# Kernel tuning notes

Measured on AMD Instinct MI355X. Metric: run time of the kernel, lower is better.

The kernel has to match this reference:

```python
import jax, jax.numpy as jnp
import numpy as np

D_KEY = 128
INF = 1e9  # stands in for the module's global INF constant


def setup_inputs() -> dict:
    key = jax.random.key(0)
    kq, kk, kv = jax.random.split(key, 3)
    B, S, D = 8, 4096, D_KEY
    return {
        "query": jax.random.normal(kq, (B, S, D), dtype=jnp.float32),
        "keys": jax.random.normal(kk, (B, S, D), dtype=jnp.float32),
        "values": jax.random.normal(kv, (B, S, D), dtype=jnp.float32),
    }


def reference(query, keys, values):
    # dot_products: [B, Sq, Sk]
    scores = jnp.einsum("bqd,bkd->bqk", query, keys)
    S = scores.shape[-1]
    # causal: subtract INF on strict upper triangle (triu(1)), applied BEFORE scaling
    causal = jnp.triu(jnp.ones((S, S), dtype=scores.dtype), 1) * INF
    logits = (scores - causal[None, :, :]) / jnp.asarray(np.sqrt(D_KEY), scores.dtype)
    # legacy F.softmax on 3D transposed tensor == softmax over key axis
    probs = jax.nn.softmax(logits, axis=-1)
    # dropout with p=0.0 is identity
    return jnp.einsum("bqk,bkd->bqd", probs, values)
```

## Files before the change

kernel.cpp:

```cpp
#include <hip/hip_runtime.h>
#include <hip/hip_bf16.h>

#define B_SZ   8
#define S_LEN  4096
#define D_K    128
#define KB     64
#define CH     16
#define NCHUNK 1280

#define KT_STR 136
#define VT_STR 72
#define PT_STR 72

typedef short  short8  __attribute__((ext_vector_type(8)));
typedef float  floatx4 __attribute__((ext_vector_type(4)));

#define EXP2F(x) exp2f(x)

__device__ __forceinline__ unsigned bfround(float x) {
  unsigned u = __builtin_bit_cast(unsigned, x);
  return (u + 0x7fffu + ((u >> 16) & 1u)) >> 16;
}
__device__ __forceinline__ unsigned bfpack2(float a, float b) {
  return bfround(a) | (bfround(b) << 16);
}


__global__ __launch_bounds__(256)
void conv_k(const float* __restrict__ K, unsigned short* __restrict__ Kb) {
  const size_t idx = ((size_t)blockIdx.x * 256 + threadIdx.x) * 8;
  float4 f0 = *(const float4*)(K + idx);
  float4 f1 = *(const float4*)(K + idx + 4);
  uint4 u;
  u.x = bfpack2(f0.x, f0.y);
  u.y = bfpack2(f0.z, f0.w);
  u.z = bfpack2(f1.x, f1.y);
  u.w = bfpack2(f1.z, f1.w);
  *(uint4*)(Kb + idx) = u;
}

__global__ __launch_bounds__(256)
void transp_v(const float* __restrict__ V, unsigned short* __restrict__ Vt) {
  __shared__ float tile[64][65];
  const int t   = threadIdx.x;
  const int bid = blockIdx.x;
  const int b   = bid >> 7;
  const int rem = bid & 127;
  const int kt  = (rem >> 1) * 64;
  const int dt  = (rem & 1) * 64;
  {
    const int c  = (t & 15) * 4;
    const int r0 = t >> 4;
#pragma unroll
    for (int rr = 0; rr < 4; ++rr) {
      const int r = r0 + rr * 16;
      float4 f = *(const float4*)(V + (size_t)(b * S_LEN + kt + r) * D_K + dt + c);
      tile[r][c]     = f.x;
      tile[r][c + 1] = f.y;
      tile[r][c + 2] = f.z;
      tile[r][c + 3] = f.w;
    }
  }
  __syncthreads();
  {
    const int d  = t >> 2;
    const int k0 = (t & 3) * 16;
#pragma unroll
    for (int j = 0; j < 16; j += 8) {
      uint4 u;
      u.x = bfpack2(tile[k0 + j + 0][d], tile[k0 + j + 1][d]);
      u.y = bfpack2(tile[k0 + j + 2][d], tile[k0 + j + 3][d]);
      u.z = bfpack2(tile[k0 + j + 4][d], tile[k0 + j + 5][d]);
      u.w = bfpack2(tile[k0 + j + 6][d], tile[k0 + j + 7][d]);
      *(uint4*)(Vt + (size_t)(b * D_K + dt + d) * S_LEN + kt + k0 + j) = u;
    }
  }
}

__global__ void zero_cnt(int* cnt) { *cnt = 0; }


__global__ __launch_bounds__(128, 2)
void attn_worker(const float* __restrict__ Q, const unsigned short* __restrict__ Kb,
                 const unsigned short* __restrict__ Vt, int* __restrict__ cnt,
                 float* __restrict__ ml, float* __restrict__ pO) {
  __shared__ __align__(16) short Klds[KB * KT_STR];
  __shared__ __align__(16) short Vtlds[D_K * VT_STR];
  __shared__ __align__(16) short Plds[2 * 16 * PT_STR];
  __shared__ int s_chunk;

  const int tid  = threadIdx.x;
  const int lane = tid & 63;
  const int w    = tid >> 6;
  const int l15  = lane & 15;
  const int quad = lane >> 4;

  const int kr0 = tid >> 4;
  const int kc  = (tid & 15) * 8;
  const int vr0 = tid >> 3;
  const int vc  = (tid & 7) * 8;

  const float CSC = 0.12752041f;

  for (;;) {
    if (tid == 0) s_chunk = atomicAdd(cnt, 1);
    __syncthreads();
    const int c = s_chunk;
    if (c >= NCHUNK) break;

    int b, qi, j;
    if (c < 800) {
      const int r = c >> 3;  b = c & 7;
      if      (r <  4) { qi = 63;               j = r;            }
      else if (r < 52) { qi = 62 - (r-4)/3;     j = (r-4)%3;      }
      else if (r < 84) { qi = 46 - (r-52)/2;    j = (r-52)%2;     }
      else             { qi = 30 - (r-84);      j = 0;            }
    } else {
      const int rc = c - 800;
      const int s  = 15 - (rc >> 5);
      const int t  = rc & 31;
      b  = t & 7;
      qi = s - 1 + 16 * (t >> 3);
      j  = (qi + 1) >> 4;
    }

    const int q0 = qi * 64;
    const int s0 = j * CH;
    const int s1 = min(s0 + CH, qi + 1);

    short8 bq[2][4];
    int qg[2];
#pragma unroll
    for (int sub = 0; sub < 2; ++sub) {
      qg[sub] = q0 + w * 32 + sub * 16 + l15;
      const float* qrow = Q + (size_t)(b * S_LEN + qg[sub]) * D_K + quad * 8;
#pragma unroll
      for (int kd = 0; kd < 4; ++kd) {
        float4 f0 = *(const float4*)(qrow + kd * 32);
        float4 f1 = *(const float4*)(qrow + kd * 32 + 4);
        union { short8 s; unsigned u[4]; } t;
        t.u[0] = bfpack2(f0.x, f0.y);
        t.u[1] = bfpack2(f0.z, f0.w);
        t.u[2] = bfpack2(f1.x, f1.y);
        t.u[3] = bfpack2(f1.z, f1.w);
        bq[sub][kd] = t.s;
      }
    }

    floatx4 acc[2][8];
#pragma unroll
    for (int sub = 0; sub < 2; ++sub)
#pragma unroll
      for (int nc = 0; nc < 8; ++nc) acc[sub][nc] = (floatx4){0.f, 0.f, 0.f, 0.f};
    float m_run[2] = {-1e30f, -1e30f}, l_run[2] = {0.f, 0.f};

    const unsigned short* kbase = Kb + (size_t)(b * S_LEN) * D_K;
    const unsigned short* vbase = Vt + (size_t)(b * D_K) * S_LEN;

    for (int s = s0; s < s1; ++s) {
      const int kt = s * KB;

#pragma unroll
      for (int i = 0; i < 8; ++i) {
        uint4 u = *(const uint4*)(kbase + (size_t)(kt + kr0 + i * 8) * D_K + kc);
        *(uint4*)(&Klds[(kr0 + i * 8) * KT_STR + kc]) = u;
      }
#pragma unroll
      for (int i = 0; i < 8; ++i) {
        uint4 u = *(const uint4*)(vbase + (size_t)(vr0 + i * 16) * S_LEN + kt + vc);
        *(uint4*)(&Vtlds[(vr0 + i * 16) * VT_STR + vc]) = u;
      }
      __syncthreads();

      floatx4 st[2][4];
#pragma unroll
      for (int kf = 0; kf < 4; ++kf) {
        floatx4 c0 = (floatx4){0.f, 0.f, 0.f, 0.f};
        floatx4 c1 = (floatx4){0.f, 0.f, 0.f, 0.f};
#pragma unroll
        for (int kd = 0; kd < 4; ++kd) {
          short8 a = *(const short8*)(&Klds[(kf * 16 + l15) * KT_STR + kd * 32 + quad * 8]);
          c0 = __builtin_amdgcn_mfma_f32_16x16x32_bf16(a, bq[0][kd], c0, 0, 0, 0);
          c1 = __builtin_amdgcn_mfma_f32_16x16x32_bf16(a, bq[1][kd], c1, 0, 0, 0);
        }
        st[0][kf] = c0;
        st[1][kf] = c1;
      }

      if (s == qi) {
#pragma unroll
        for (int sub = 0; sub < 2; ++sub)
#pragma unroll
          for (int kf = 0; kf < 4; ++kf)
#pragma unroll
            for (int r = 0; r < 4; ++r) {
              int key = kt + kf * 16 + quad * 4 + r;
              if (key > qg[sub]) st[sub][kf][r] = -1e30f;
            }
      }

      short8 pa[2][2];
#pragma unroll
      for (int sub = 0; sub < 2; ++sub) {
        float mx = st[sub][0][0];
#pragma unroll
        for (int kf = 0; kf < 4; ++kf)
#pragma unroll
          for (int r = 0; r < 4; ++r) mx = fmaxf(mx, st[sub][kf][r]);
        mx = fmaxf(mx, __shfl_xor(mx, 16, 64));
        mx = fmaxf(mx, __shfl_xor(mx, 32, 64));
        const float m_new = fmaxf(m_run[sub], mx);
        const float alpha = EXP2F((m_run[sub] - m_new) * CSC);

        float p[4][4];
        float tsum = 0.f;
#pragma unroll
        for (int kf = 0; kf < 4; ++kf)
#pragma unroll
          for (int r = 0; r < 4; ++r) {
            p[kf][r] = EXP2F((st[sub][kf][r] - m_new) * CSC);
            tsum += p[kf][r];
          }
        tsum += __shfl_xor(tsum, 16, 64);
        tsum += __shfl_xor(tsum, 32, 64);
        l_run[sub] = l_run[sub] * alpha + tsum;
        m_run[sub] = m_new;

#pragma unroll
        for (int r = 0; r < 4; ++r) {
          const float ar = __shfl(alpha, quad * 4 + r, 64);
#pragma unroll
          for (int nc = 0; nc < 8; ++nc) acc[sub][nc][r] *= ar;
        }

        short* pw = &Plds[(w * 16 + l15) * PT_STR];
#pragma unroll
        for (int kf = 0; kf < 4; ++kf) {
          uint2 u;
          u.x = bfpack2(p[kf][0], p[kf][1]);
          u.y = bfpack2(p[kf][2], p[kf][3]);
          *(uint2*)(&pw[kf * 16 + quad * 4]) = u;
        }
        __asm__ __volatile__("" ::: "memory");
        pa[sub][0] = *(const short8*)(&pw[quad * 8]);
        pa[sub][1] = *(const short8*)(&pw[32 + quad * 8]);
        __asm__ __volatile__("" ::: "memory");
      }

#pragma unroll
      for (int nc = 0; nc < 8; ++nc) {
        short8 bv0 = *(const short8*)(&Vtlds[(nc * 16 + l15) * VT_STR + quad * 8]);
        short8 bv1 = *(const short8*)(&Vtlds[(nc * 16 + l15) * VT_STR + 32 + quad * 8]);
        acc[0][nc] = __builtin_amdgcn_mfma_f32_16x16x32_bf16(pa[0][0], bv0, acc[0][nc], 0, 0, 0);
        acc[0][nc] = __builtin_amdgcn_mfma_f32_16x16x32_bf16(pa[0][1], bv1, acc[0][nc], 0, 0, 0);
        acc[1][nc] = __builtin_amdgcn_mfma_f32_16x16x32_bf16(pa[1][0], bv0, acc[1][nc], 0, 0, 0);
        acc[1][nc] = __builtin_amdgcn_mfma_f32_16x16x32_bf16(pa[1][1], bv1, acc[1][nc], 0, 0, 0);
      }
      __syncthreads();
    }

    const int slot = ((b << 6) | qi) * 4 + j;
    float* po = pO + (size_t)slot * 8192;
#pragma unroll
    for (int sub = 0; sub < 2; ++sub) {
#pragma unroll
      for (int r = 0; r < 4; ++r) {
        const int qrow = w * 32 + sub * 16 + quad * 4 + r;
        float* op = po + qrow * D_K + l15;
#pragma unroll
        for (int nc = 0; nc < 8; ++nc) op[nc * 16] = acc[sub][nc][r];
      }
      if (quad == 0) {
        const int qrow = w * 32 + sub * 16 + l15;
        ml[(size_t)slot * 128 + qrow * 2]     = m_run[sub];
        ml[(size_t)slot * 128 + qrow * 2 + 1] = l_run[sub];
      }
    }
  }
}


__global__ __launch_bounds__(256)
void attn_combine(const float* __restrict__ ml, const float* __restrict__ pO,
                  float* __restrict__ O) {
  const int t   = blockIdx.x;
  const int b   = t >> 6;
  const int qi  = t & 63;
  const int ncb = ((qi + 1) + 15) >> 4;
  const float CSC = 0.12752041f;

  const int tid = threadIdx.x;
  const int q   = tid >> 2;
  const int dp  = (tid & 3) * 32;

  float m[4], l[4];
  float M = -1e30f;
  for (int jj = 0; jj < ncb; ++jj) {
    const int slot = t * 4 + jj;
    m[jj] = ml[(size_t)slot * 128 + q * 2];
    l[jj] = ml[(size_t)slot * 128 + q * 2 + 1];
    M = fmaxf(M, m[jj]);
  }
  float wgt[4], L = 0.f;
  for (int jj = 0; jj < ncb; ++jj) {
    wgt[jj] = EXP2F((m[jj] - M) * CSC);
    L += wgt[jj] * l[jj];
  }
  const float inv = 1.0f / L;

  float4 out[8];
#pragma unroll
  for (int v = 0; v < 8; ++v) out[v] = make_float4(0.f, 0.f, 0.f, 0.f);
  for (int jj = 0; jj < ncb; ++jj) {
    const float* src = pO + (size_t)(t * 4 + jj) * 8192 + q * D_K + dp;
    const float wj = wgt[jj];
#pragma unroll
    for (int v = 0; v < 8; ++v) {
      float4 f = *(const float4*)(src + v * 4);
      out[v].x += wj * f.x;  out[v].y += wj * f.y;
      out[v].z += wj * f.z;  out[v].w += wj * f.w;
    }
  }
  float* dst = O + (size_t)(b * S_LEN + qi * 64 + q) * D_K + dp;
#pragma unroll
  for (int v = 0; v < 8; ++v) {
    float4 f = make_float4(out[v].x * inv, out[v].y * inv, out[v].z * inv, out[v].w * inv);
    *(float4*)(dst + v * 4) = f;
  }
}


__global__ __launch_bounds__(256, 2)
void attn_fwd_fb(const float* __restrict__ Q, const float* __restrict__ K,
                 const float* __restrict__ V, float* __restrict__ O) {
  __shared__ __align__(16) short Klds[KB * KT_STR];
  __shared__ __align__(16) short Vtlds[D_K * VT_STR];
  __shared__ __align__(16) short Plds[4 * 16 * PT_STR];

  const int tid  = threadIdx.x;
  const int lane = tid & 63;
  const int w    = tid >> 6;
  const int l15  = lane & 15;
  const int quad = lane >> 4;

  const int bid = blockIdx.x;
  const int b   = bid & 7;
  const int qi  = 63 - (bid >> 3);
  const int q0  = qi * 64;

  const float CSC = 0.12752041f;

  const int    qg   = q0 + w * 16 + l15;
  const float* qrow = Q + (size_t)(b * S_LEN + qg) * D_K + quad * 8;
  short8 bq[4];
#pragma unroll
  for (int kd = 0; kd < 4; ++kd) {
    float4 f0 = *(const float4*)(qrow + kd * 32);
    float4 f1 = *(const float4*)(qrow + kd * 32 + 4);
    union { short8 s; unsigned u[4]; } t;
    t.u[0] = bfpack2(f0.x, f0.y);
    t.u[1] = bfpack2(f0.z, f0.w);
    t.u[2] = bfpack2(f1.x, f1.y);
    t.u[3] = bfpack2(f1.z, f1.w);
    bq[kd] = t.s;
  }

  floatx4 acc[8];
#pragma unroll
  for (int nc = 0; nc < 8; ++nc) acc[nc] = (floatx4){0.f, 0.f, 0.f, 0.f};
  float m_run = -1e30f, l_run = 0.f;

  const int d4 = tid & 31;
  const int kq = tid >> 5;
  const int nsteps = qi + 1;

  for (int s = 0; s < nsteps; ++s) {
    const int kt = s * KB;
#pragma unroll
    for (int r2 = 0; r2 < 2; ++r2) {
      const int row = r2 * 32 + kq * 4;
      const float* kp = K + (size_t)(b * S_LEN + kt + row) * D_K + d4 * 4;
      const float* vp = V + (size_t)(b * S_LEN + kt + row) * D_K + d4 * 4;
      float4 fk[4], fv[4];
#pragma unroll
      for (int i = 0; i < 4; ++i) {
        fk[i] = *(const float4*)(kp + i * D_K);
        fv[i] = *(const float4*)(vp + i * D_K);
      }
#pragma unroll
      for (int i = 0; i < 4; ++i) {
        uint2 u;
        u.x = bfpack2(fk[i].x, fk[i].y);
        u.y = bfpack2(fk[i].z, fk[i].w);
        *(uint2*)(&Klds[(row + i) * KT_STR + d4 * 4]) = u;
      }
#pragma unroll
      for (int c = 0; c < 4; ++c) {
        float e0 = ((const float*)&fv[0])[c];
        float e1 = ((const float*)&fv[1])[c];
        float e2 = ((const float*)&fv[2])[c];
        float e3 = ((const float*)&fv[3])[c];
        uint2 u;
        u.x = bfpack2(e0, e1);
        u.y = bfpack2(e2, e3);
        *(uint2*)(&Vtlds[(d4 * 4 + c) * VT_STR + row]) = u;
      }
    }
    __syncthreads();

    floatx4 st[4];
#pragma unroll
    for (int kf = 0; kf < 4; ++kf) {
      floatx4 c = (floatx4){0.f, 0.f, 0.f, 0.f};
#pragma unroll
      for (int kd = 0; kd < 4; ++kd) {
        short8 a = *(const short8*)(&Klds[(kf * 16 + l15) * KT_STR + kd * 32 + quad * 8]);
        c = __builtin_amdgcn_mfma_f32_16x16x32_bf16(a, bq[kd], c, 0, 0, 0);
      }
      st[kf] = c;
    }

    if (s == nsteps - 1) {
#pragma unroll
      for (int kf = 0; kf < 4; ++kf)
#pragma unroll
        for (int r = 0; r < 4; ++r) {
          int key = kt + kf * 16 + quad * 4 + r;
          if (key > qg) st[kf][r] = -1e30f;
        }
    }

    float mx = st[0][0];
#pragma unroll
    for (int kf = 0; kf < 4; ++kf)
#pragma unroll
      for (int r = 0; r < 4; ++r) mx = fmaxf(mx, st[kf][r]);
    mx = fmaxf(mx, __shfl_xor(mx, 16, 64));
    mx = fmaxf(mx, __shfl_xor(mx, 32, 64));
    const float m_new = fmaxf(m_run, mx);
    const float alpha = EXP2F((m_run - m_new) * CSC);

    float p[4][4];
    float tsum = 0.f;
#pragma unroll
    for (int kf = 0; kf < 4; ++kf)
#pragma unroll
      for (int r = 0; r < 4; ++r) {
        p[kf][r] = EXP2F((st[kf][r] - m_new) * CSC);
        tsum += p[kf][r];
      }
    tsum += __shfl_xor(tsum, 16, 64);
    tsum += __shfl_xor(tsum, 32, 64);
    l_run = l_run * alpha + tsum;
    m_run = m_new;

#pragma unroll
    for (int r = 0; r < 4; ++r) {
      const float ar = __shfl(alpha, quad * 4 + r, 64);
#pragma unroll
      for (int nc = 0; nc < 8; ++nc) acc[nc][r] *= ar;
    }

    short* pw = &Plds[(w * 16 + l15) * PT_STR];
#pragma unroll
    for (int kf = 0; kf < 4; ++kf) {
      uint2 u;
      u.x = bfpack2(p[kf][0], p[kf][1]);
      u.y = bfpack2(p[kf][2], p[kf][3]);
      *(uint2*)(&pw[kf * 16 + quad * 4]) = u;
    }
    __asm__ __volatile__("" ::: "memory");
    short8 pa0 = *(const short8*)(&pw[quad * 8]);
    short8 pa1 = *(const short8*)(&pw[32 + quad * 8]);

#pragma unroll
    for (int nc = 0; nc < 8; ++nc) {
      short8 bv0 = *(const short8*)(&Vtlds[(nc * 16 + l15) * VT_STR + quad * 8]);
      acc[nc] = __builtin_amdgcn_mfma_f32_16x16x32_bf16(pa0, bv0, acc[nc], 0, 0, 0);
      short8 bv1 = *(const short8*)(&Vtlds[(nc * 16 + l15) * VT_STR + 32 + quad * 8]);
      acc[nc] = __builtin_amdgcn_mfma_f32_16x16x32_bf16(pa1, bv1, acc[nc], 0, 0, 0);
    }
    __syncthreads();
  }

#pragma unroll
  for (int r = 0; r < 4; ++r) {
    const float lr  = __shfl(l_run, quad * 4 + r, 64);
    const float inv = 1.0f / lr;
    const int qout  = q0 + w * 16 + quad * 4 + r;
    float* op = O + (size_t)(b * S_LEN + qout) * D_K + l15;
#pragma unroll
    for (int nc = 0; nc < 8; ++nc) op[nc * 16] = acc[nc][r] * inv;
  }
}


extern "C" void kernel_launch(void* const* d_in, const int* in_sizes, int n_in,
                              void* d_out, int out_size, void* d_ws, size_t ws_size,
                              hipStream_t stream) {
  const float* Q = (const float*)d_in[0];
  const float* K = (const float*)d_in[1];
  const float* V = (const float*)d_in[2];
  float* O = (float*)d_out;

  const size_t elems = (size_t)B_SZ * S_LEN * D_K;

  const size_t off_ml = 256;
  const size_t off_po = off_ml + 2048ull * 128 * 4;
  const size_t off_kb = off_po + 2048ull * 8192 * 4;
  const size_t off_vt = off_kb + elems * 2;
  const size_t need   = off_vt + elems * 2;

  if (ws_size >= need) {
    char* ws = (char*)d_ws;
    int*            cnt = (int*)ws;
    float*          ml  = (float*)(ws + off_ml);
    float*          po  = (float*)(ws + off_po);
    unsigned short* Kb  = (unsigned short*)(ws + off_kb);
    unsigned short* Vt  = (unsigned short*)(ws + off_vt);

    zero_cnt<<<dim3(1), dim3(1), 0, stream>>>(cnt);
    conv_k<<<dim3((unsigned)(elems / 8 / 256)), dim3(256), 0, stream>>>(K, Kb);
    transp_v<<<dim3(B_SZ * (S_LEN / 64) * (D_K / 64)), dim3(256), 0, stream>>>(V, Vt);
    attn_worker<<<dim3(1024), dim3(128), 0, stream>>>(Q, Kb, Vt, cnt, ml, po);
    attn_combine<<<dim3(512), dim3(256), 0, stream>>>(ml, po, O);
  } else {
    attn_fwd_fb<<<dim3(512), dim3(256), 0, stream>>>(Q, K, V, O);
  }
}
```

Baseline: 195.3 us.

## Restructure split-K attention: static chunk grid, 128-row tiles, prefetch, fused prep

Drops the atomic work-queue scheduler in favour of a static grid of 768 chunks. Each 256-thread block now covers a 128-query tile and up to 13 key tiles. K/V tiles for the next step are prefetched into registers while the current step computes. The separate K-conversion and V-transpose kernels are merged into one prep kernel, and the counter-reset kernel is removed. Waves whose rows lie fully above the causal diagonal skip work, and accumulator rescaling is skipped when the running max does not grow. Packing now uses the hardware v_cvt_pk_bf16_f32 instruction. Losing dynamic balancing and using larger blocks may cause tail imbalance, and the larger register footprint could limit occupancy.

```diff
diff --git a/kernel.cpp b/kernel.cpp
--- a/kernel.cpp
+++ b/kernel.cpp
@@ -1,12 +1,11 @@
 #include <hip/hip_runtime.h>
-#include <hip/hip_bf16.h>
 
 #define B_SZ   8
 #define S_LEN  4096
 #define D_K    128
 #define KB     64
-#define CH     16
-#define NCHUNK 1280
+#define CH     13
+#define NCHUNK 768
 
 #define KT_STR 136
 #define VT_STR 72
@@ -16,6 +15,7 @@
 typedef float  floatx4 __attribute__((ext_vector_type(4)));
 
 #define EXP2F(x) exp2f(x)
+#define NCH(q) ((2*(q) + 14) / 13)
 
 __device__ __forceinline__ unsigned bfround(float x) {
   unsigned u = __builtin_bit_cast(unsigned, x);
@@ -24,70 +24,74 @@
 __device__ __forceinline__ unsigned bfpack2(float a, float b) {
   return bfround(a) | (bfround(b) << 16);
 }
+__device__ __forceinline__ unsigned cvtpk(float lo, float hi) {
+  unsigned r;
+  asm("v_cvt_pk_bf16_f32 %0, %1, %2" : "=v"(r) : "v"(lo), "v"(hi));
+  return r;
+}
 
 
 __global__ __launch_bounds__(256)
-void conv_k(const float* __restrict__ K, unsigned short* __restrict__ Kb) {
-  const size_t idx = ((size_t)blockIdx.x * 256 + threadIdx.x) * 8;
-  float4 f0 = *(const float4*)(K + idx);
-  float4 f1 = *(const float4*)(K + idx + 4);
-  uint4 u;
-  u.x = bfpack2(f0.x, f0.y);
-  u.y = bfpack2(f0.z, f0.w);
-  u.z = bfpack2(f1.x, f1.y);
-  u.w = bfpack2(f1.z, f1.w);
-  *(uint4*)(Kb + idx) = u;
-}
-
-__global__ __launch_bounds__(256)
-void transp_v(const float* __restrict__ V, unsigned short* __restrict__ Vt) {
+void prep(const float* __restrict__ K, const float* __restrict__ V,
+          unsigned short* __restrict__ Kb, unsigned short* __restrict__ Vt) {
+  const int tid = threadIdx.x;
+  const int bid = blockIdx.x;
+
+#pragma unroll
+  for (int it = 0; it < 2; ++it) {
+    const size_t idx = (size_t)bid * 4096 + it * 2048 + tid * 8;
+    float4 f0 = *(const float4*)(K + idx);
+    float4 f1 = *(const float4*)(K + idx + 4);
+    uint4 u;
+    u.x = bfpack2(f0.x, f0.y);
+    u.y = bfpack2(f0.z, f0.w);
+    u.z = bfpack2(f1.x, f1.y);
+    u.w = bfpack2(f1.z, f1.w);
+    *(uint4*)(Kb + idx) = u;
+  }
+
   __shared__ float tile[64][65];
-  const int t   = threadIdx.x;
-  const int bid = blockIdx.x;
-  const int b   = bid >> 7;
+  const int vb  = bid >> 7;
   const int rem = bid & 127;
-  const int kt  = (rem >> 1) * 64;
+  const int ktt = (rem >> 1) * 64;
   const int dt  = (rem & 1) * 64;
   {
-    const int c  = (t & 15) * 4;
-    const int r0 = t >> 4;
-#pragma unroll
-    for (int rr = 0; rr < 4; ++rr) {
-      const int r = r0 + rr * 16;
-      float4 f = *(const float4*)(V + (size_t)(b * S_LEN + kt + r) * D_K + dt + c);
-      tile[r][c]     = f.x;
-      tile[r][c + 1] = f.y;
-      tile[r][c + 2] = f.z;
-      tile[r][c + 3] = f.w;
+    const int c  = (tid & 15) * 4;
+    const int r0 = tid >> 4;
+#pragma unroll
+    for (int rr2 = 0; rr2 < 4; ++rr2) {
+      const int rr = r0 + rr2 * 16;
+      float4 f = *(const float4*)(V + (size_t)(vb * S_LEN + ktt + rr) * D_K + dt + c);
+      tile[rr][c]     = f.x;
+      tile[rr][c + 1] = f.y;
+      tile[rr][c + 2] = f.z;
+      tile[rr][c + 3] = f.w;
     }
   }
   __syncthreads();
   {
-    const int d  = t >> 2;
-    const int k0 = (t & 3) * 16;
-#pragma unroll
-    for (int j = 0; j < 16; j += 8) {
+    const int d  = tid >> 2;
+    const int k0 = (tid & 3) * 16;
+#pragma unroll
+    for (int jj = 0; jj < 16; jj += 8) {
       uint4 u;
-      u.x = bfpack2(tile[k0 + j + 0][d], tile[k0 + j + 1][d]);
-      u.y = bfpack2(tile[k0 + j + 2][d], tile[k0 + j + 3][d]);
-      u.z = bfpack2(tile[k0 + j + 4][d], tile[k0 + j + 5][d]);
-      u.w = bfpack2(tile[k0 + j + 6][d], tile[k0 + j + 7][d]);
-      *(uint4*)(Vt + (size_t)(b * D_K + dt + d) * S_LEN + kt + k0 + j) = u;
-    }
-  }
-}
-
-__global__ void zero_cnt(int* cnt) { *cnt = 0; }
-
-
-__global__ __launch_bounds__(128, 2)
+      u.x = bfpack2(tile[k0 + jj + 0][d], tile[k0 + jj + 1][d]);
+      u.y = bfpack2(tile[k0 + jj + 2][d], tile[k0 + jj + 3][d]);
+      u.z = bfpack2(tile[k0 + jj + 4][d], tile[k0 + jj + 5][d]);
+      u.w = bfpack2(tile[k0 + jj + 6][d], tile[k0 + jj + 7][d]);
+      *(uint4*)(Vt + (size_t)(vb * D_K + dt + d) * S_LEN + ktt + k0 + jj) = u;
+    }
+  }
+}
+
+
+__global__ __launch_bounds__(256, 3)
 void attn_worker(const float* __restrict__ Q, const unsigned short* __restrict__ Kb,
-                 const unsigned short* __restrict__ Vt, int* __restrict__ cnt,
+                 const unsigned short* __restrict__ Vt,
                  float* __restrict__ ml, float* __restrict__ pO) {
   __shared__ __align__(16) short Klds[KB * KT_STR];
   __shared__ __align__(16) short Vtlds[D_K * VT_STR];
-  __shared__ __align__(16) short Plds[2 * 16 * PT_STR];
-  __shared__ int s_chunk;
+  __shared__ __align__(16) short Plds[4 * 16 * PT_STR];
 
   const int tid  = threadIdx.x;
   const int lane = tid & 63;
@@ -95,84 +99,81 @@
   const int l15  = lane & 15;
   const int quad = lane >> 4;
 
-  const int kr0 = tid >> 4;
-  const int kc  = (tid & 15) * 8;
-  const int vr0 = tid >> 3;
-  const int vc  = (tid & 7) * 8;
+  const int cidx = blockIdx.x;
+  const int b = cidx & 7;
+  int q = 31, r = cidx >> 3;
+  while (r >= NCH(q)) { r -= NCH(q); --q; }
+  const int j  = r;
+  const int q0 = q * 128;
+  const int s0 = j * CH;
+  const int s1 = min(s0 + CH, 2 * q + 2);
+
+  const int kr  = tid >> 2;
+  const int kc2 = (tid & 3) * 32;
+  const int vr  = tid >> 1;
+  const int vc2 = (tid & 1) * 32;
 
   const float CSC = 0.12752041f;
 
-  for (;;) {
-    if (tid == 0) s_chunk = atomicAdd(cnt, 1);
-    __syncthreads();
-    const int c = s_chunk;
-    if (c >= NCHUNK) break;
-
-    int b, qi, j;
-    if (c < 800) {
-      const int r = c >> 3;  b = c & 7;
-      if      (r <  4) { qi = 63;               j = r;            }
-      else if (r < 52) { qi = 62 - (r-4)/3;     j = (r-4)%3;      }
-      else if (r < 84) { qi = 46 - (r-52)/2;    j = (r-52)%2;     }
-      else             { qi = 30 - (r-84);      j = 0;            }
-    } else {
-      const int rc = c - 800;
-      const int s  = 15 - (rc >> 5);
-      const int t  = rc & 31;
-      b  = t & 7;
-      qi = s - 1 + 16 * (t >> 3);
-      j  = (qi + 1) >> 4;
-    }
-
-    const int q0 = qi * 64;
-    const int s0 = j * CH;
-    const int s1 = min(s0 + CH, qi + 1);
-
-    short8 bq[2][4];
-    int qg[2];
-#pragma unroll
-    for (int sub = 0; sub < 2; ++sub) {
-      qg[sub] = q0 + w * 32 + sub * 16 + l15;
-      const float* qrow = Q + (size_t)(b * S_LEN + qg[sub]) * D_K + quad * 8;
-#pragma unroll
-      for (int kd = 0; kd < 4; ++kd) {
-        float4 f0 = *(const float4*)(qrow + kd * 32);
-        float4 f1 = *(const float4*)(qrow + kd * 32 + 4);
-        union { short8 s; unsigned u[4]; } t;
-        t.u[0] = bfpack2(f0.x, f0.y);
-        t.u[1] = bfpack2(f0.z, f0.w);
-        t.u[2] = bfpack2(f1.x, f1.y);
-        t.u[3] = bfpack2(f1.z, f1.w);
-        bq[sub][kd] = t.s;
-      }
-    }
-
-    floatx4 acc[2][8];
-#pragma unroll
-    for (int sub = 0; sub < 2; ++sub)
-#pragma unroll
-      for (int nc = 0; nc < 8; ++nc) acc[sub][nc] = (floatx4){0.f, 0.f, 0.f, 0.f};
-    float m_run[2] = {-1e30f, -1e30f}, l_run[2] = {0.f, 0.f};
-
-    const unsigned short* kbase = Kb + (size_t)(b * S_LEN) * D_K;
-    const unsigned short* vbase = Vt + (size_t)(b * D_K) * S_LEN;
-
-    for (int s = s0; s < s1; ++s) {
-      const int kt = s * KB;
-
-#pragma unroll
-      for (int i = 0; i < 8; ++i) {
-        uint4 u = *(const uint4*)(kbase + (size_t)(kt + kr0 + i * 8) * D_K + kc);
-        *(uint4*)(&Klds[(kr0 + i * 8) * KT_STR + kc]) = u;
-      }
-#pragma unroll
-      for (int i = 0; i < 8; ++i) {
-        uint4 u = *(const uint4*)(vbase + (size_t)(vr0 + i * 16) * S_LEN + kt + vc);
-        *(uint4*)(&Vtlds[(vr0 + i * 16) * VT_STR + vc]) = u;
-      }
-      __syncthreads();
-
-      floatx4 st[2][4];
+  short8 bq[2][4];
+  int qg[2];
+#pragma unroll
+  for (int sub = 0; sub < 2; ++sub) {
+    qg[sub] = q0 + w * 32 + sub * 16 + l15;
+    const float* qptr = Q + (size_t)(b * S_LEN + qg[sub]) * D_K + quad * 8;
+#pragma unroll
+    for (int kd = 0; kd < 4; ++kd) {
+      float4 f0 = *(const float4*)(qptr + kd * 32);
+      float4 f1 = *(const float4*)(qptr + kd * 32 + 4);
+      union { short8 s; unsigned u[4]; } t;
+      t.u[0] = cvtpk(f0.x, f0.y);
+      t.u[1] = cvtpk(f0.z, f0.w);
+      t.u[2] = cvtpk(f1.x, f1.y);
+      t.u[3] = cvtpk(f1.z, f1.w);
+      bq[sub][kd] = t.s;
+    }
+  }
+
+  floatx4 acc[2][8];
+#pragma unroll
+  for (int sub = 0; sub < 2; ++sub)
+#pragma unroll
+    for (int nc = 0; nc < 8; ++nc) acc[sub][nc] = (floatx4){0.f, 0.f, 0.f, 0.f};
+  float m_run[2] = {-1e30f, -1e30f}, l_run[2] = {0.f, 0.f};
+
+  const unsigned short* kb0 = Kb + (size_t)b * S_LEN * D_K;
+  const unsigned short* vb0 = Vt + (size_t)b * D_K * S_LEN;
+
+  uint4 kpf[4], vpf[4];
+
+  {
+    const unsigned short* kp = kb0 + (size_t)(s0 * KB) * D_K;
+    const unsigned short* vp = vb0 + s0 * KB;
+#pragma unroll
+    for (int i = 0; i < 4; ++i) kpf[i] = *(const uint4*)(kp + (size_t)kr * D_K + kc2 + i * 8);
+#pragma unroll
+    for (int i = 0; i < 4; ++i) vpf[i] = *(const uint4*)(vp + (size_t)vr * S_LEN + vc2 + i * 8);
+#pragma unroll
+    for (int i = 0; i < 4; ++i) *(uint4*)(&Klds[kr * KT_STR + kc2 + i * 8]) = kpf[i];
+#pragma unroll
+    for (int i = 0; i < 4; ++i) *(uint4*)(&Vtlds[vr * VT_STR + vc2 + i * 8]) = vpf[i];
+  }
+  __syncthreads();
+
+  for (int s = s0; s < s1; ++s) {
+    const int kt  = s * KB;
+    const bool hn  = (s + 1 < s1);
+    const bool act = (kt <= q0 + w * 32 + 31);
+
+    if (hn) {
+      const unsigned short* kp = kb0 + (size_t)((s + 1) * KB) * D_K;
+#pragma unroll
+      for (int i = 0; i < 4; ++i) kpf[i] = *(const uint4*)(kp + (size_t)kr * D_K + kc2 + i * 8);
+    }
+
+    floatx4 st[2][4];
+    short8 pa[2][2];
+    if (act) {
 #pragma unroll
       for (int kf = 0; kf < 4; ++kf) {
         floatx4 c0 = (floatx4){0.f, 0.f, 0.f, 0.f};
@@ -187,58 +188,61 @@
         st[1][kf] = c1;
       }
 
-      if (s == qi) {
-#pragma unroll
-        for (int sub = 0; sub < 2; ++sub)
+#pragma unroll
+      for (int sub = 0; sub < 2; ++sub) {
+        if (kt + 63 > q0 + w * 32 + sub * 16) {
 #pragma unroll
           for (int kf = 0; kf < 4; ++kf)
 #pragma unroll
-            for (int r = 0; r < 4; ++r) {
-              int key = kt + kf * 16 + quad * 4 + r;
-              if (key > qg[sub]) st[sub][kf][r] = -1e30f;
+            for (int rr = 0; rr < 4; ++rr) {
+              int key = kt + kf * 16 + quad * 4 + rr;
+              if (key > qg[sub]) st[sub][kf][rr] = -1e30f;
             }
-      }
-
-      short8 pa[2][2];
+        }
+      }
+
 #pragma unroll
       for (int sub = 0; sub < 2; ++sub) {
         float mx = st[sub][0][0];
 #pragma unroll
         for (int kf = 0; kf < 4; ++kf)
 #pragma unroll
-          for (int r = 0; r < 4; ++r) mx = fmaxf(mx, st[sub][kf][r]);
+          for (int rr = 0; rr < 4; ++rr) mx = fmaxf(mx, st[sub][kf][rr]);
         mx = fmaxf(mx, __shfl_xor(mx, 16, 64));
         mx = fmaxf(mx, __shfl_xor(mx, 32, 64));
         const float m_new = fmaxf(m_run[sub], mx);
-        const float alpha = EXP2F((m_run[sub] - m_new) * CSC);
+        const bool  grow  = __any(m_new > m_run[sub]);
+        const float alpha = grow ? EXP2F((m_run[sub] - m_new) * CSC) : 1.0f;
 
         float p[4][4];
         float tsum = 0.f;
 #pragma unroll
         for (int kf = 0; kf < 4; ++kf)
 #pragma unroll
-          for (int r = 0; r < 4; ++r) {
-            p[kf][r] = EXP2F((st[sub][kf][r] - m_new) * CSC);
-            tsum += p[kf][r];
+          for (int rr = 0; rr < 4; ++rr) {
+            p[kf][rr] = EXP2F((st[sub][kf][rr] - m_new) * CSC);
+            tsum += p[kf][rr];
           }
         tsum += __shfl_xor(tsum, 16, 64);
         tsum += __shfl_xor(tsum, 32, 64);
         l_run[sub] = l_run[sub] * alpha + tsum;
         m_run[sub] = m_new;
 
-#pragma unroll
-        for (int r = 0; r < 4; ++r) {
-          const float ar = __shfl(alpha, quad * 4 + r, 64);
-#pragma unroll
-          for (int nc = 0; nc < 8; ++nc) acc[sub][nc][r] *= ar;
+        if (grow) {
+#pragma unroll
+          for (int rr = 0; rr < 4; ++rr) {
+            const float ar = __shfl(alpha, quad * 4 + rr, 64);
+#pragma unroll
+            for (int nc = 0; nc < 8; ++nc) acc[sub][nc][rr] *= ar;
+          }
         }
 
         short* pw = &Plds[(w * 16 + l15) * PT_STR];
 #pragma unroll
         for (int kf = 0; kf < 4; ++kf) {
           uint2 u;
-          u.x = bfpack2(p[kf][0], p[kf][1]);
-          u.y = bfpack2(p[kf][2], p[kf][3]);
+          u.x = cvtpk(p[kf][0], p[kf][1]);
+          u.y = cvtpk(p[kf][2], p[kf][3]);
           *(uint2*)(&pw[kf * 16 + quad * 4]) = u;
         }
         __asm__ __volatile__("" ::: "memory");
@@ -246,7 +250,15 @@
         pa[sub][1] = *(const short8*)(&pw[32 + quad * 8]);
         __asm__ __volatile__("" ::: "memory");
       }
-
+    }
+
+    if (hn) {
+      const unsigned short* vp = vb0 + (s + 1) * KB;
+#pragma unroll
+      for (int i = 0; i < 4; ++i) vpf[i] = *(const uint4*)(vp + (size_t)vr * S_LEN + vc2 + i * 8);
+    }
+
+    if (act) {
 #pragma unroll
       for (int nc = 0; nc < 8; ++nc) {
         short8 bv0 = *(const short8*)(&Vtlds[(nc * 16 + l15) * VT_STR + quad * 8]);
@@ -256,25 +268,33 @@
         acc[1][nc] = __builtin_amdgcn_mfma_f32_16x16x32_bf16(pa[1][0], bv0, acc[1][nc], 0, 0, 0);
         acc[1][nc] = __builtin_amdgcn_mfma_f32_16x16x32_bf16(pa[1][1], bv1, acc[1][nc], 0, 0, 0);
       }
+    }
+
+    __syncthreads();
+    if (hn) {
+#pragma unroll
+      for (int i = 0; i < 4; ++i) *(uint4*)(&Klds[kr * KT_STR + kc2 + i * 8]) = kpf[i];
+#pragma unroll
+      for (int i = 0; i < 4; ++i) *(uint4*)(&Vtlds[vr * VT_STR + vc2 + i * 8]) = vpf[i];
       __syncthreads();
     }
-
-    const int slot = ((b << 6) | qi) * 4 + j;
-    float* po = pO + (size_t)slot * 8192;
-#pragma unroll
-    for (int sub = 0; sub < 2; ++sub) {
-#pragma unroll
-      for (int r = 0; r < 4; ++r) {
-        const int qrow = w * 32 + sub * 16 + quad * 4 + r;
-        float* op = po + qrow * D_K + l15;
-#pragma unroll
-        for (int nc = 0; nc < 8; ++nc) op[nc * 16] = acc[sub][nc][r];
-      }
-      if (quad == 0) {
-        const int qrow = w * 32 + sub * 16 + l15;
-        ml[(size_t)slot * 128 + qrow * 2]     = m_run[sub];
-        ml[(size_t)slot * 128 + qrow * 2 + 1] = l_run[sub];
-      }
+  }
+
+  const int slot = cidx;
+  float* po = pO + (size_t)slot * 16384;
+#pragma unroll
+  for (int sub = 0; sub < 2; ++sub) {
+#pragma unroll
+    for (int rr = 0; rr < 4; ++rr) {
+      const int qrow = w * 32 + sub * 16 + quad * 4 + rr;
+      float* op = po + qrow * D_K + l15;
+#pragma unroll
+      for (int nc = 0; nc < 8; ++nc) op[nc * 16] = acc[sub][nc][rr];
+    }
+    if (quad == 0) {
+      const int qrow = w * 32 + sub * 16 + l15;
+      ml[(size_t)slot * 256 + qrow * 2]     = m_run[sub];
+      ml[(size_t)slot * 256 + qrow * 2 + 1] = l_run[sub];
     }
   }
 }
@@ -283,49 +303,57 @@
 __global__ __launch_bounds__(256)
 void attn_combine(const float* __restrict__ ml, const float* __restrict__ pO,
                   float* __restrict__ O) {
-  const int t   = blockIdx.x;
-  const int b   = t >> 6;
-  const int qi  = t & 63;
-  const int ncb = ((qi + 1) + 15) >> 4;
+  const int t = blockIdx.x;
+  const int b = t & 7;
+  const int q = t >> 3;
+  int D = 0;
+  for (int tq = 31; tq > q; --tq) D += NCH(tq);
+  const int ncb = NCH(q);
   const float CSC = 0.12752041f;
 
   const int tid = threadIdx.x;
-  const int q   = tid >> 2;
-  const int dp  = (tid & 3) * 32;
-
-  float m[4], l[4];
+  const int ql  = tid >> 1;
+  const int dh  = (tid & 1) * 64;
+
+  float m[5], l[5], wgt[5];
   float M = -1e30f;
-  for (int jj = 0; jj < ncb; ++jj) {
-    const int slot = t * 4 + jj;
-    m[jj] = ml[(size_t)slot * 128 + q * 2];
-    l[jj] = ml[(size_t)slot * 128 + q * 2 + 1];
-    M = fmaxf(M, m[jj]);
-  }
-  float wgt[4], L = 0.f;
-  for (int jj = 0; jj < ncb; ++jj) {
-    wgt[jj] = EXP2F((m[jj] - M) * CSC);
-    L += wgt[jj] * l[jj];
-  }
+#pragma unroll
+  for (int jj = 0; jj < 5; ++jj) {
+    if (jj < ncb) {
+      const size_t slot = (size_t)(D + jj) * 8 + b;
+      m[jj] = ml[slot * 256 + ql * 2];
+      l[jj] = ml[slot * 256 + ql * 2 + 1];
+      M = fmaxf(M, m[jj]);
+    }
+  }
+  float L = 0.f;
+#pragma unroll
+  for (int jj = 0; jj < 5; ++jj)
+    if (jj < ncb) { wgt[jj] = EXP2F((m[jj] - M) * CSC); L += wgt[jj] * l[jj]; }
   const float inv = 1.0f / L;
 
-  float4 out[8];
-#pragma unroll
-  for (int v = 0; v < 8; ++v) out[v] = make_float4(0.f, 0.f, 0.f, 0.f);
-  for (int jj = 0; jj < ncb; ++jj) {
-    const float* src = pO + (size_t)(t * 4 + jj) * 8192 + q * D_K + dp;
-    const float wj = wgt[jj];
-#pragma unroll
-    for (int v = 0; v < 8; ++v) {
-      float4 f = *(const float4*)(src + v * 4);
-      out[v].x += wj * f.x;  out[v].y += wj * f.y;
-      out[v].z += wj * f.z;  out[v].w += wj * f.w;
-    }
-  }
-  float* dst = O + (size_t)(b * S_LEN + qi * 64 + q) * D_K + dp;
-#pragma unroll
-  for (int v = 0; v < 8; ++v) {
-    float4 f = make_float4(out[v].x * inv, out[v].y * inv, out[v].z * inv, out[v].w * inv);
-    *(float4*)(dst + v * 4) = f;
+  float4 out[16];
+#pragma unroll
+  for (int v = 0; v < 16; ++v) out[v] = make_float4(0.f, 0.f, 0.f, 0.f);
+#pragma unroll
+  for (int jj = 0; jj < 5; ++jj) {
+    if (jj < ncb) {
+      const size_t slot = (size_t)(D + jj) * 8 + b;
+      const float* src = pO + slot * 16384 + ql * D_K + dh;
+      const float wj = wgt[jj];
+#pragma unroll
+      for (int v = 0; v < 16; ++v) {
+        float4 f = *(const float4*)(src + v * 4);
+        out[v].x += wj * f.x;  out[v].y += wj * f.y;
+        out[v].z += wj * f.z;  out[v].w += wj * f.w;
+      }
+    }
+  }
+  float* dst = O + ((size_t)(b * S_LEN) + q * 128 + ql) * D_K + dh;
+#pragma unroll
+  for (int v = 0; v < 16; ++v) {
+    *(float4*)(dst + v * 4) = make_float4(out[v].x * inv, out[v].y * inv,
+                                          out[v].z * inv, out[v].w * inv);
   }
 }
 
@@ -424,9 +452,9 @@
 #pragma unroll
       for (int kf = 0; kf < 4; ++kf)
 #pragma unroll
-        for (int r = 0; r < 4; ++r) {
-          int key = kt + kf * 16 + quad * 4 + r;
-          if (key > qg) st[kf][r] = -1e30f;
+        for (int rr = 0; rr < 4; ++rr) {
+          int key = kt + kf * 16 + quad * 4 + rr;
+          if (key > qg) st[kf][rr] = -1e30f;
         }
     }
 
@@ -434,7 +462,7 @@
 #pragma unroll
     for (int kf = 0; kf < 4; ++kf)
 #pragma unroll
-      for (int r = 0; r < 4; ++r) mx = fmaxf(mx, st[kf][r]);
+      for (int rr = 0; rr < 4; ++rr) mx = fmaxf(mx, st[kf][rr]);
     mx = fmaxf(mx, __shfl_xor(mx, 16, 64));
     mx = fmaxf(mx, __shfl_xor(mx, 32, 64));
     const float m_new = fmaxf(m_run, mx);
@@ -445,9 +473,9 @@
 #pragma unroll
     for (int kf = 0; kf < 4; ++kf)
 #pragma unroll
-      for (int r = 0; r < 4; ++r) {
-        p[kf][r] = EXP2F((st[kf][r] - m_new) * CSC);
-        tsum += p[kf][r];
+      for (int rr = 0; rr < 4; ++rr) {
+        p[kf][rr] = EXP2F((st[kf][rr] - m_new) * CSC);
+        tsum += p[kf][rr];
       }
     tsum += __shfl_xor(tsum, 16, 64);
     tsum += __shfl_xor(tsum, 32, 64);
@@ -455,10 +483,10 @@
     m_run = m_new;
 
 #pragma unroll
-    for (int r = 0; r < 4; ++r) {
-      const float ar = __shfl(alpha, quad * 4 + r, 64);
-#pragma unroll
-      for (int nc = 0; nc < 8; ++nc) acc[nc][r] *= ar;
+    for (int rr = 0; rr < 4; ++rr) {
+      const float ar = __shfl(alpha, quad * 4 + rr, 64);
+#pragma unroll
+      for (int nc = 0; nc < 8; ++nc) acc[nc][rr] *= ar;
     }
 
     short* pw = &Plds[(w * 16 + l15) * PT_STR];
@@ -484,13 +512,13 @@
   }
 
 #pragma unroll
-  for (int r = 0; r < 4; ++r) {
-    const float lr  = __shfl(l_run, quad * 4 + r, 64);
+  for (int rr = 0; rr < 4; ++rr) {
+    const float lr  = __shfl(l_run, quad * 4 + rr, 64);
     const float inv = 1.0f / lr;
-    const int qout  = q0 + w * 16 + quad * 4 + r;
+    const int qout  = q0 + w * 16 + quad * 4 + rr;
     float* op = O + (size_t)(b * S_LEN + qout) * D_K + l15;
 #pragma unroll
-    for (int nc = 0; nc < 8; ++nc) op[nc * 16] = acc[nc][r] * inv;
+    for (int nc = 0; nc < 8; ++nc) op[nc * 16] = acc[nc][rr] * inv;
   }
 }
 
@@ -505,25 +533,22 @@
 
   const size_t elems = (size_t)B_SZ * S_LEN * D_K;
 
-  const size_t off_ml = 256;
-  const size_t off_po = off_ml + 2048ull * 128 * 4;
-  const size_t off_kb = off_po + 2048ull * 8192 * 4;
+  const size_t off_ml = 0;
+  const size_t off_po = (size_t)NCHUNK * 256 * 4;
+  const size_t off_kb = off_po + (size_t)NCHUNK * 16384 * 4;
   const size_t off_vt = off_kb + elems * 2;
   const size_t need   = off_vt + elems * 2;
 
   if (ws_size >= need) {
     char* ws = (char*)d_ws;
-    int*            cnt = (int*)ws;
-    float*          ml  = (float*)(ws + off_ml);
+    float*          mlp = (float*)(ws + off_ml);
     float*          po  = (float*)(ws + off_po);
     unsigned short* Kb  = (unsigned short*)(ws + off_kb);
     unsigned short* Vt  = (unsigned short*)(ws + off_vt);
 
-    zero_cnt<<<dim3(1), dim3(1), 0, stream>>>(cnt);
-    conv_k<<<dim3((unsigned)(elems / 8 / 256)), dim3(256), 0, stream>>>(K, Kb);
-    transp_v<<<dim3(B_SZ * (S_LEN / 64) * (D_K / 64)), dim3(256), 0, stream>>>(V, Vt);
-    attn_worker<<<dim3(1024), dim3(128), 0, stream>>>(Q, Kb, Vt, cnt, ml, po);
-    attn_combine<<<dim3(512), dim3(256), 0, stream>>>(ml, po, O);
+    prep<<<dim3(1024), dim3(256), 0, stream>>>(K, V, Kb, Vt);
+    attn_worker<<<dim3(NCHUNK), dim3(256), 0, stream>>>(Q, Kb, Vt, mlp, po);
+    attn_combine<<<dim3(256), dim3(256), 0, stream>>>(mlp, po, O);
   } else {
     attn_fwd_fb<<<dim3(512), dim3(256), 0, stream>>>(Q, K, V, O);
   }
```

After: 213.3 us. 9.2% more time.
